# Kernel optimization log

Hardware: AMD Instinct MI355X
Metric: run time of the kernel (lower is better)

## Reference

```python
import jax, jax.numpy as jnp
import numpy as np

N_DRUG, N_CELL, N_GENE = 2048, 2048, 4096
N = N_DRUG + N_CELL + N_GENE
E = 262144
H1, H2, H3, HEADS = 256, 64, 64, 4
N_PAIRS = 10000
EPS = 1e-5


def _gatv2(x, src, dst, Wl, bl, Wr, br, att, bias, heads, out_ch):
    # PyG GATv2Conv: e_ij = att . leaky_relu(Wl x_j + Wr x_i), softmax over incoming edges of i,
    # out_i = sum_j alpha_ij * (Wl x_j), heads concatenated, plus output bias.
    n = x.shape[0]
    xl = (x @ Wl + bl).reshape(n, heads, out_ch)   # source transform
    xr = (x @ Wr + br).reshape(n, heads, out_ch)   # target transform
    e = jax.nn.leaky_relu(xl[src] + xr[dst], 0.2)  # [E, H, C]
    logits = jnp.einsum('ehc,hc->eh', e, att)      # [E, H]
    m = jax.ops.segment_max(logits, dst, num_segments=n)
    ex = jnp.exp(logits - m[dst])
    denom = jax.ops.segment_sum(ex, dst, num_segments=n)
    alpha = ex / denom[dst]                        # [E, H]
    out = jax.ops.segment_sum(xl[src] * alpha[:, :, None], dst, num_segments=n)
    return out.reshape(n, heads * out_ch) + bias, alpha


def _graph_norm(x, gamma, beta, mscale):
    # PyG GraphNorm over a single graph: out = (x - a*mean) / sqrt(var + eps) * gamma + beta
    mu = x.mean(0)
    sub = x - mu * mscale
    var = (sub * sub).mean(0)
    return sub / jnp.sqrt(var + EPS) * gamma + beta


def setup_inputs() -> dict:
    key = jax.random.key(0)
    ks = jax.random.split(key, 24)
    f = jnp.float32
    nrm = lambda k, shape, sc: jax.random.normal(k, shape, f) * sc
    drug = jax.random.normal(ks[0], (N_DRUG, N_DRUG), f)
    cell = jax.random.normal(ks[1], (N_CELL, N_CELL), f)
    gene = jax.random.normal(ks[2], (N_GENE, N_GENE), f)
    # random edges guaranteed to have no self loops (PyG would remove then re-add them)
    src = jax.random.randint(ks[3], (E,), 0, N)
    off = jax.random.randint(ks[4], (E,), 1, N)
    edges = jnp.stack([src, (src + off) % N]).astype(jnp.int32)
    idx_drug = jax.random.randint(ks[5], (N_PAIRS,), 0, N_DRUG)
    idx_cell = N_DRUG + jax.random.randint(ks[6], (N_PAIRS,), 0, N_CELL)
    HC2, HC3 = HEADS * H2, HEADS * H3
    return {
        'drug': drug, 'cell': cell, 'gene': gene,
        'edges': edges, 'idx_drug': idx_drug, 'idx_cell': idx_cell,
        'W_drug': nrm(ks[7], (N_DRUG, H1), 1 / np.sqrt(N_DRUG)), 'b_drug': jnp.zeros((H1,), f),
        'W_cell': nrm(ks[8], (N_CELL, H1), 1 / np.sqrt(N_CELL)), 'b_cell': jnp.zeros((H1,), f),
        'W_gene': nrm(ks[9], (N_GENE, H1), 1 / np.sqrt(N_GENE)), 'b_gene': jnp.zeros((H1,), f),
        'gat1_Wl': nrm(ks[10], (H1, HC2), 1 / np.sqrt(H1)), 'gat1_bl': jnp.zeros((HC2,), f),
        'gat1_Wr': nrm(ks[11], (H1, HC2), 1 / np.sqrt(H1)), 'gat1_br': jnp.zeros((HC2,), f),
        'gat1_att': nrm(ks[12], (HEADS, H2), 1 / np.sqrt(H2)), 'gat1_bias': jnp.zeros((HC2,), f),
        'gat2_Wl': nrm(ks[13], (HC2, HC3), 1 / np.sqrt(HC2)), 'gat2_bl': jnp.zeros((HC3,), f),
        'gat2_Wr': nrm(ks[14], (HC2, HC3), 1 / np.sqrt(HC2)), 'gat2_br': jnp.zeros((HC3,), f),
        'gat2_att': nrm(ks[15], (HEADS, H3), 1 / np.sqrt(H3)), 'gat2_bias': jnp.zeros((HC3,), f),
        'gn1_gamma': jnp.ones((HC2,), f), 'gn1_beta': jnp.zeros((HC2,), f), 'gn1_scale': jnp.ones((HC2,), f),
        'gn2_gamma': jnp.ones((HC3,), f), 'gn2_beta': jnp.zeros((HC3,), f), 'gn2_scale': jnp.ones((HC3,), f),
        'lin1_W': nrm(ks[16], (2 * HC3, 1), 1 / np.sqrt(2 * HC3)), 'lin1_b': jnp.zeros((1,), f),
    }


def reference(drug, cell, gene, edges, idx_drug, idx_cell,
              W_drug, b_drug, W_cell, b_cell, W_gene, b_gene,
              gat1_Wl, gat1_bl, gat1_Wr, gat1_br, gat1_att, gat1_bias,
              gat2_Wl, gat2_bl, gat2_Wr, gat2_br, gat2_att, gat2_bias,
              gn1_gamma, gn1_beta, gn1_scale, gn2_gamma, gn2_beta, gn2_scale,
              lin1_W, lin1_b):
    x = jnp.concatenate([drug @ W_drug + b_drug,
                         cell @ W_cell + b_cell,
                         gene @ W_gene + b_gene], axis=0)  # [N, H1]
    loops = jnp.arange(N, dtype=edges.dtype)
    src = jnp.concatenate([edges[0], loops])  # GATv2Conv adds self loops
    dst = jnp.concatenate([edges[1], loops])
    x, a1 = _gatv2(x, src, dst, gat1_Wl, gat1_bl, gat1_Wr, gat1_br, gat1_att, gat1_bias, HEADS, H2)
    x = jax.nn.relu(_graph_norm(x, gn1_gamma, gn1_beta, gn1_scale))  # dropout = identity (eval)
    x, a2 = _gatv2(x, src, dst, gat2_Wl, gat2_bl, gat2_Wr, gat2_br, gat2_att, gat2_bias, HEADS, H3)
    x = jax.nn.relu(_graph_norm(x, gn2_gamma, gn2_beta, gn2_scale))
    pair = jnp.concatenate([x[idx_drug], x[idx_cell]], axis=1)  # [P, 2*H*H3]
    pred = jax.nn.sigmoid(pair @ lin1_W + lin1_b)
    # get_attention_mat: dense [N,N], every edge position set to the (detached) scalar mean of
    # attention weights; the two layer matrices share edge positions so they simply add.
    val = jax.lax.stop_gradient(a1.mean() + a2.mean())
    attn = jnp.zeros((N, N), x.dtype).at[src, dst].set(val)
    return pred, attn
```

## Files before the change

kernel.cpp:

```cpp
#include <hip/hip_runtime.h>

#define NNODES 8192
#define NEDGE  262144
#define EETOT  270336
#define NPAIRS 10000

typedef __attribute__((ext_vector_type(8))) short s16x8;
typedef __attribute__((ext_vector_type(8))) unsigned short u16x8;
typedef __attribute__((ext_vector_type(4))) float f32x4;

__device__ __forceinline__ float lrelu(float v) { return v > 0.f ? v : 0.2f * v; }

__device__ __forceinline__ void split2(float a, unsigned short& h, unsigned short& l) {
  unsigned u = __float_as_uint(a);
  h = (unsigned short)(u >> 16);
  float hf = __uint_as_float(u & 0xffff0000u);
  float r = a - hf;
  unsigned v = __float_as_uint(r);
  v += 0x7fffu + ((v >> 16) & 1u);
  l = (unsigned short)(v >> 16);
}

__device__ __forceinline__ unsigned short f2bf(float f) {
  unsigned u = __float_as_uint(f);
  u += 0x7fffu + ((u >> 16) & 1u);
  return (unsigned short)(u >> 16);
}
__device__ __forceinline__ float bf2f(unsigned short u) {
  return __uint_as_float((unsigned)u << 16);
}

__device__ __forceinline__ void wsplit_body(const float* __restrict__ W,
    unsigned short* __restrict__ Th, int K, int blk) {
  int col = threadIdx.x;
  int kb = blk * 8;
  u16x8 vh;
#pragma unroll
  for (int i = 0; i < 8; ++i)
    vh[i] = f2bf(W[(size_t)(kb + i) * 256 + col]);
  *(u16x8*)(Th + (size_t)col * K + kb) = vh;
}

__global__ __launch_bounds__(256) void k_wsplit_all(
    const float* __restrict__ Wd, const float* __restrict__ Wc, const float* __restrict__ Wg,
    const float* __restrict__ W1l, const float* __restrict__ W1r,
    const float* __restrict__ W2l, const float* __restrict__ W2r,
    unsigned short* __restrict__ tdh, unsigned short* __restrict__ tch,
    unsigned short* __restrict__ tgh,
    unsigned short* __restrict__ tl1h, unsigned short* __restrict__ tr1h,
    unsigned short* __restrict__ tl2h, unsigned short* __restrict__ tr2h,
    int* __restrict__ counts_d, int* __restrict__ counts_s, float* __restrict__ stats) {
  int b = blockIdx.x;
  if      (b < 256)  wsplit_body(Wd,  tdh, 2048, b);
  else if (b < 512)  wsplit_body(Wc,  tch, 2048, b - 256);
  else if (b < 1024) wsplit_body(Wg,  tgh, 4096, b - 512);
  else if (b < 1056) { wsplit_body(W1l, tl1h, 256, b - 1024);
                       counts_d[(b - 1024) * 256 + threadIdx.x] = 0; }
  else if (b < 1088) { wsplit_body(W1r, tr1h, 256, b - 1056);
                       counts_s[(b - 1056) * 256 + threadIdx.x] = 0; }
  else if (b < 1120) { wsplit_body(W2l, tl2h, 256, b - 1088);
                       if (b < 1092) stats[(b - 1088) * 256 + threadIdx.x] = 0.f; }
  else               wsplit_body(W2r, tr2h, 256, b - 1120);
}

struct Tile128 {
  unsigned short Ah[128][40], Al[128][40], Bh[128][40];
};
struct TileN {
  Tile128 t;
  float nsc[256], nsh[256];
};

template<bool BIAS, bool OUTBF, bool NORM>
__device__ __forceinline__ void gemm_tile128(Tile128& s,
    const float* __restrict__ A, int lda,
    const unsigned short* __restrict__ Th, int ldb, int nsteps,
    const float* __restrict__ bias, float* __restrict__ C,
    unsigned short* __restrict__ Cb,
    const float* __restrict__ nsc, const float* __restrict__ nsh) {
  const int tid = threadIdx.x;
  const int wave = tid >> 6, lane = tid & 63;
  const int g = lane >> 4, r = lane & 15;
  const int wr = (wave >> 1) * 64, wc = (wave & 1) * 64;

  const int ar = tid >> 1, ak = (tid & 1) * 16;
  const float* Arow = A + (size_t)ar * lda + ak;
  const int bc = tid & 127, bk = (tid >> 7) * 16;
  const unsigned short* Bhs = Th + (size_t)bc * ldb + bk;

  f32x4 acc[4][4];
#pragma unroll
  for (int m = 0; m < 4; ++m)
#pragma unroll
    for (int n = 0; n < 4; ++n)
#pragma unroll
      for (int j = 0; j < 4; ++j) acc[m][n][j] = 0.f;

  float4 pa0 = *(const float4*)(Arow);
  float4 pa1 = *(const float4*)(Arow + 4);
  float4 pa2 = *(const float4*)(Arow + 8);
  float4 pa3 = *(const float4*)(Arow + 12);
  u16x8 ph0 = *(const u16x8*)(Bhs);
  u16x8 ph1 = *(const u16x8*)(Bhs + 8);

  for (int t = 0; t < nsteps; ++t) {
    {
      float av[16] = {pa0.x, pa0.y, pa0.z, pa0.w, pa1.x, pa1.y, pa1.z, pa1.w,
                      pa2.x, pa2.y, pa2.z, pa2.w, pa3.x, pa3.y, pa3.z, pa3.w};
      u16x8 vh0, vh1, vl0, vl1;
#pragma unroll
      for (int i = 0; i < 16; ++i) {
        float v = av[i];
        if constexpr (NORM) {
          int ch = t * 32 + ak + i;
          v = fmaxf(v * nsc[ch] + nsh[ch], 0.f);
        }
        unsigned short hh, ll;
        split2(v, hh, ll);
        if (i < 8) { vh0[i] = hh; vl0[i] = ll; }
        else       { vh1[i - 8] = hh; vl1[i - 8] = ll; }
      }
      *(u16x8*)&s.Ah[ar][ak]     = vh0;
      *(u16x8*)&s.Ah[ar][ak + 8] = vh1;
      *(u16x8*)&s.Al[ar][ak]     = vl0;
      *(u16x8*)&s.Al[ar][ak + 8] = vl1;
      *(u16x8*)&s.Bh[bc][bk]     = ph0;
      *(u16x8*)&s.Bh[bc][bk + 8] = ph1;
    }
    __syncthreads();
    if (t + 1 < nsteps) {
      const float* An = Arow + (size_t)(t + 1) * 32;
      pa0 = *(const float4*)(An);
      pa1 = *(const float4*)(An + 4);
      pa2 = *(const float4*)(An + 8);
      pa3 = *(const float4*)(An + 12);
      const unsigned short* Bhn = Bhs + (size_t)(t + 1) * 32;
      ph0 = *(const u16x8*)(Bhn);
      ph1 = *(const u16x8*)(Bhn + 8);
    }
    s16x8 fah[4], fal[4], fbh[4];
#pragma unroll
    for (int m = 0; m < 4; ++m) {
      fah[m] = *(const s16x8*)&s.Ah[wr + m * 16 + r][g * 8];
      fal[m] = *(const s16x8*)&s.Al[wr + m * 16 + r][g * 8];
    }
#pragma unroll
    for (int n = 0; n < 4; ++n)
      fbh[n] = *(const s16x8*)&s.Bh[wc + n * 16 + r][g * 8];
#pragma unroll
    for (int m = 0; m < 4; ++m)
#pragma unroll
      for (int n = 0; n < 4; ++n) {
        acc[m][n] = __builtin_amdgcn_mfma_f32_16x16x32_bf16(fal[m], fbh[n], acc[m][n], 0, 0, 0);
        acc[m][n] = __builtin_amdgcn_mfma_f32_16x16x32_bf16(fah[m], fbh[n], acc[m][n], 0, 0, 0);
      }
    __syncthreads();
  }
#pragma unroll
  for (int m = 0; m < 4; ++m)
#pragma unroll
    for (int n = 0; n < 4; ++n) {
      int col = wc + n * 16 + r;
      float bv = BIAS ? bias[col] : 0.f;
      int rowb = wr + m * 16 + g * 4;
#pragma unroll
      for (int j = 0; j < 4; ++j) {
        float v = acc[m][n][j] + bv;
        if constexpr (OUTBF) Cb[(size_t)(rowb + j) * 256 + col] = f2bf(v);
        else                 C[(size_t)(rowb + j) * 256 + col] = v;
      }
    }
}

#define PDRUG_PLANE ((size_t)2048 * 256)
#define PGENE_PLANE ((size_t)4096 * 256)
__global__ __launch_bounds__(256) void k_inproj_fill(
    const float* __restrict__ drug, const float* __restrict__ cell,
    const float* __restrict__ gene,
    const unsigned short* __restrict__ tdh, const unsigned short* __restrict__ tch,
    const unsigned short* __restrict__ tgh, float* __restrict__ P,
    const int* __restrict__ csrdst, const int* __restrict__ rowst_s,
    float* __restrict__ attn) {
  __shared__ Tile128 s;
  int b = blockIdx.x;
  if (b >= 768) {
    int row = b - 768;
    float* rp = attn + (size_t)row * NNODES;
    f32x4* p4 = (f32x4*)rp;
    f32x4 z = {0.f, 0.f, 0.f, 0.f};
#pragma unroll
    for (int j = 0; j < 8; ++j)
      __builtin_nontemporal_store(z, p4 + j * 256 + threadIdx.x);
    __syncthreads();
    int e0 = rowst_s[row], e1 = rowst_s[row + 1];
    for (int j = e0 + (int)threadIdx.x; j < e1; j += 256)
      rp[csrdst[j]] = 16384.0f / 270336.0f;
    return;
  }
  if (b < 256) {
    int idx = b & 127;
    int colblk = (idx >> 3) & 1;
    int rest = (idx & 7) | ((idx >> 4) << 3);
    int rowblk = rest >> 2, chunk = rest & 3;
    const float* X = (b < 128) ? drug : cell;
    const unsigned short* Th = (b < 128) ? tdh : tch;
    float* Pb = P + ((b < 128) ? 0 : 4 * PDRUG_PLANE);
    gemm_tile128<false, false, false>(s,
        X + (size_t)rowblk * 128 * 2048 + (size_t)chunk * 512, 2048,
        Th + (size_t)colblk * 128 * 2048 + chunk * 512, 2048, 16, nullptr,
        Pb + (size_t)chunk * PDRUG_PLANE + (size_t)rowblk * 128 * 256 + colblk * 128,
        nullptr, nullptr, nullptr);
  } else {
    int idx = b - 256;
    int colblk = (idx >> 3) & 1;
    int rest = (idx & 7) | ((idx >> 4) << 3);
    int rowblk = rest >> 3, chunk = rest & 7;
    gemm_tile128<false, false, false>(s,
        gene + (size_t)rowblk * 128 * 4096 + (size_t)chunk * 512, 4096,
        tgh + (size_t)colblk * 128 * 4096 + chunk * 512, 4096, 16, nullptr,
        P + 8 * PDRUG_PLANE + (size_t)chunk * PGENE_PLANE + (size_t)rowblk * 128 * 256 + colblk * 128,
        nullptr, nullptr, nullptr);
  }
}

__global__ __launch_bounds__(256) void k_reduce(const float* __restrict__ P,
    const float* __restrict__ bd, const float* __restrict__ bc,
    const float* __restrict__ bg, float* __restrict__ out) {
  int idx = blockIdx.x * 256 + threadIdx.x;
  size_t e = (size_t)idx * 4;
  int row = (int)(e >> 8);
  int col = (int)(e & 255);
  const float* base; const float* bias; size_t plane; int np;
  if (row < 2048) {
    base = P + (size_t)row * 256 + col; bias = bd; plane = PDRUG_PLANE; np = 4;
  } else if (row < 4096) {
    base = P + 4 * PDRUG_PLANE + (size_t)(row - 2048) * 256 + col; bias = bc;
    plane = PDRUG_PLANE; np = 4;
  } else {
    base = P + 8 * PDRUG_PLANE + (size_t)(row - 4096) * 256 + col; bias = bg;
    plane = PGENE_PLANE; np = 8;
  }
  float4 s = *(const float4*)(base);
  for (int p = 1; p < np; ++p) {
    float4 v = *(const float4*)(base + p * plane);
    s.x += v.x; s.y += v.y; s.z += v.z; s.w += v.w;
  }
  float4 bv = *(const float4*)(bias + col);
  s.x += bv.x; s.y += bv.y; s.z += bv.z; s.w += bv.w;
  *(float4*)(out + e) = s;
}

template<bool NORM>
__global__ __launch_bounds__(256) void k_gemm2(const float* __restrict__ A,
    const unsigned short* __restrict__ ThL, const unsigned short* __restrict__ ThR,
    const float* __restrict__ biasL, const float* __restrict__ biasR,
    unsigned short* __restrict__ CLb, float* __restrict__ CR,
    const float* __restrict__ csum, const float* __restrict__ csumsq,
    const float* __restrict__ gamma, const float* __restrict__ beta,
    const float* __restrict__ mscale) {
  __shared__ TileN s;
  int b = blockIdx.x;
  int sub = (b >> 3) & 3;
  int x = (b & 7) | ((b >> 5) << 3);
  if constexpr (NORM) {
    int c = threadIdx.x;
    float mu = csum[c] * (1.0f / 8192.0f);
    float ex2 = csumsq[c] * (1.0f / 8192.0f);
    float smu = mscale[c] * mu;
    float var = ex2 - 2.f * smu * mu + smu * smu;
    float sc = rsqrtf(var + 1e-5f) * gamma[c];
    s.nsc[c] = sc;
    s.nsh[c] = beta[c] - smu * sc;
    __syncthreads();
  }
  int row0 = x * 128;
  int col0 = (sub & 1) * 128;
  if (sub >= 2) {
    gemm_tile128<true, false, NORM>(s.t, A + (size_t)row0 * 256, 256,
        ThR + (size_t)col0 * 256, 256, 8,
        biasR + col0, CR + (size_t)row0 * 256 + col0, nullptr, s.nsc, s.nsh);
  } else {
    gemm_tile128<true, true, NORM>(s.t, A + (size_t)row0 * 256, 256,
        ThL + (size_t)col0 * 256, 256, 8,
        biasL + col0, nullptr, CLb + (size_t)row0 * 256 + col0, s.nsc, s.nsh);
  }
}

__global__ void k_count2(const int* __restrict__ edges, int* __restrict__ cd,
                         int* __restrict__ cs) {
  int e = blockIdx.x * blockDim.x + threadIdx.x;
  if (e >= EETOT) return;
  int s, d;
  if (e < NEDGE) { s = edges[e]; d = edges[NEDGE + e]; } else { s = d = e - NEDGE; }
  atomicAdd(&cd[d], 1);
  atomicAdd(&cs[s], 1);
}

__global__ __launch_bounds__(1024) void k_scan2(
    const int* __restrict__ c0, int* __restrict__ r0, int* __restrict__ u0,
    const int* __restrict__ c1, int* __restrict__ r1, int* __restrict__ u1) {
  const int* counts = blockIdx.x ? c1 : c0;
  int* row_start = blockIdx.x ? r1 : r0;
  int* cursor = blockIdx.x ? u1 : u0;
  __shared__ int part[1024];
  int t = threadIdx.x;
  int base = t * 8;
  int loc[8];
  int s = 0;
#pragma unroll
  for (int j = 0; j < 8; ++j) { loc[j] = s; s += counts[base + j]; }
  part[t] = s;
  __syncthreads();
  for (int off = 1; off < 1024; off <<= 1) {
    int v = (t >= off) ? part[t - off] : 0;
    __syncthreads();
    part[t] += v;
    __syncthreads();
  }
  int pre = (t == 0) ? 0 : part[t - 1];
#pragma unroll
  for (int j = 0; j < 8; ++j) {
    int v = pre + loc[j];
    row_start[base + j] = v;
    cursor[base + j] = v;
  }
  if (t == 1023) row_start[NNODES] = pre + s;
}

__global__ void k_place2(const int* __restrict__ edges, int* __restrict__ curd,
    int* __restrict__ curs, int* __restrict__ csrsrc, int* __restrict__ csrdst) {
  int e = blockIdx.x * blockDim.x + threadIdx.x;
  if (e >= EETOT) return;
  int s, d;
  if (e < NEDGE) { s = edges[e]; d = edges[NEDGE + e]; } else { s = d = e - NEDGE; }
  int pd = atomicAdd(&curd[d], 1);
  csrsrc[pd] = s;
  int ps = atomicAdd(&curs[s], 1);
  csrdst[ps] = d;
}

__global__ __launch_bounds__(256) void k_gat(
    const unsigned short* __restrict__ xl, const float* __restrict__ xr,
    const float* __restrict__ att, const int* __restrict__ csrsrc,
    const int* __restrict__ row_start, const float* __restrict__ bias,
    float* __restrict__ out) {
  int i = blockIdx.x * 4 + (threadIdx.x >> 6);
  int lane = threadIdx.x & 63;
  int co = (lane >> 4) * 64 + (lane & 15) * 4;
  float4 w4 = *(const float4*)(att + co);
  float4 r4 = *(const float4*)(xr + (size_t)i * 256 + co);
  float sum = 0.f, ax = 0.f, ay = 0.f, az = 0.f, aw = 0.f;
  int e0 = row_start[i], e1 = row_start[i + 1];
  int deg = e1 - e0;

  for (int cb = 0; cb < deg; cb += 64) {
    int cn = min(deg - cb, 64);
    int myid = (lane < cn) ? csrsrc[e0 + cb + lane] : 0;
    auto g = [&](int j) {
      int s = __shfl(myid, j);
      return *(const ushort4*)(xl + (size_t)s * 256 + co);
    };
    ushort4 c0, c1, c2, c3, n0, n1, n2, n3;
    int curn = min(cn, 4);
    int p = 0;
    if (curn > 0) c0 = g(0);
    if (curn > 1) c1 = g(1);
    if (curn > 2) c2 = g(2);
    if (curn > 3) c3 = g(3);
    p = curn;
    for (;;) {
      int nxtn = min(cn - p, 4);
      if (nxtn > 0) n0 = g(p);
      if (nxtn > 1) n1 = g(p + 1);
      if (nxtn > 2) n2 = g(p + 2);
      if (nxtn > 3) n3 = g(p + 3);
#pragma unroll
      for (int j = 0; j < 4; ++j) {
        if (j >= curn) break;
        ushort4 u = (j == 0) ? c0 : (j == 1) ? c1 : (j == 2) ? c2 : c3;
        float x0 = bf2f(u.x), x1 = bf2f(u.y), x2 = bf2f(u.z), x3 = bf2f(u.w);
        float t = w4.x * lrelu(x0 + r4.x) + w4.y * lrelu(x1 + r4.y) +
                  w4.z * lrelu(x2 + r4.z) + w4.w * lrelu(x3 + r4.w);
        t += __shfl_xor(t, 1);
        t += __shfl_xor(t, 2);
        t += __shfl_xor(t, 4);
        t += __shfl_xor(t, 8);
        float el = __expf(fminf(t, 60.f));
        sum += el;
        ax += el * x0; ay += el * x1; az += el * x2; aw += el * x3;
      }
      if (nxtn <= 0) break;
      c0 = n0; c1 = n1; c2 = n2; c3 = n3;
      curn = nxtn; p += nxtn;
    }
  }
  float inv = 1.0f / sum;
  float4 bv = *(const float4*)(bias + co);
  float4 r;
  r.x = ax * inv + bv.x; r.y = ay * inv + bv.y;
  r.z = az * inv + bv.z; r.w = aw * inv + bv.w;
  *(float4*)(out + (size_t)i * 256 + co) = r;
}

__global__ __launch_bounds__(256) void k_colstats(const float* __restrict__ x,
    float* __restrict__ csum, float* __restrict__ csumsq) {
  int c = threadIdx.x;
  int r0 = blockIdx.x * 32;
  float s = 0.f, s2 = 0.f;
  for (int r = 0; r < 32; ++r) {
    float v = x[(size_t)(r0 + r) * 256 + c];
    s += v; s2 += v * v;
  }
  atomicAdd(&csum[c], s);
  atomicAdd(&csumsq[c], s2);
}

__global__ __launch_bounds__(256) void k_pred(const float* __restrict__ h,
    const int* __restrict__ idx_drug, const int* __restrict__ idx_cell,
    const float* __restrict__ W, const float* __restrict__ b,
    const float* __restrict__ csum, const float* __restrict__ csumsq,
    const float* __restrict__ gamma, const float* __restrict__ beta,
    const float* __restrict__ mscale, float* __restrict__ out) {
  int p = blockIdx.x * 4 + (threadIdx.x >> 6);
  if (p >= NPAIRS) return;
  int lane = threadIdx.x & 63;
  int rd = idx_drug[p], rc = idx_cell[p];
  float4 a  = *(const float4*)(h + (size_t)rd * 256 + lane * 4);
  float4 cg = *(const float4*)(h + (size_t)rc * 256 + lane * 4);
  float4 wa = *(const float4*)(W + lane * 4);
  float4 wc = *(const float4*)(W + 256 + lane * 4);
  float av[4] = {a.x, a.y, a.z, a.w};
  float cv[4] = {cg.x, cg.y, cg.z, cg.w};
  float wv[4] = {wa.x, wa.y, wa.z, wa.w};
  float uv[4] = {wc.x, wc.y, wc.z, wc.w};
  float t = 0.f;
#pragma unroll
  for (int j = 0; j < 4; ++j) {
    int ch = lane * 4 + j;
    float mu = csum[ch] * (1.0f / 8192.0f);
    float ex2 = csumsq[ch] * (1.0f / 8192.0f);
    float smu = mscale[ch] * mu;
    float var = ex2 - 2.f * smu * mu + smu * smu;
    float sc = rsqrtf(var + 1e-5f) * gamma[ch];
    float sh = beta[ch] - smu * sc;
    t += fmaxf(av[j] * sc + sh, 0.f) * wv[j] + fmaxf(cv[j] * sc + sh, 0.f) * uv[j];
  }
#pragma unroll
  for (int off = 1; off < 64; off <<= 1) t += __shfl_xor(t, off);
  if (lane == 0) out[p] = 1.0f / (1.0f + __expf(-(t + b[0])));
}

extern "C" void kernel_launch(void* const* d_in, const int* in_sizes, int n_in,
                              void* d_out, int out_size, void* d_ws, size_t ws_size,
                              hipStream_t stream) {
  const float* drug = (const float*)d_in[0];
  const float* cell = (const float*)d_in[1];
  const float* gene = (const float*)d_in[2];
  const int*   edges = (const int*)d_in[3];
  const int*   idxd = (const int*)d_in[4];
  const int*   idxc = (const int*)d_in[5];
  const float* Wd = (const float*)d_in[6];   const float* bd = (const float*)d_in[7];
  const float* Wc = (const float*)d_in[8];   const float* bc = (const float*)d_in[9];
  const float* Wg = (const float*)d_in[10];  const float* bg = (const float*)d_in[11];
  const float* g1Wl = (const float*)d_in[12]; const float* g1bl = (const float*)d_in[13];
  const float* g1Wr = (const float*)d_in[14]; const float* g1br = (const float*)d_in[15];
  const float* g1att = (const float*)d_in[16]; const float* g1bias = (const float*)d_in[17];
  const float* g2Wl = (const float*)d_in[18]; const float* g2bl = (const float*)d_in[19];
  const float* g2Wr = (const float*)d_in[20]; const float* g2br = (const float*)d_in[21];
  const float* g2att = (const float*)d_in[22]; const float* g2bias = (const float*)d_in[23];
  const float* gn1g = (const float*)d_in[24]; const float* gn1b = (const float*)d_in[25];
  const float* gn1s = (const float*)d_in[26];
  const float* gn2g = (const float*)d_in[27]; const float* gn2b = (const float*)d_in[28];
  const float* gn2s = (const float*)d_in[29];
  const float* linW = (const float*)d_in[30]; const float* linb = (const float*)d_in[31];
  float* out = (float*)d_out;
  (void)in_sizes; (void)n_in; (void)out_size; (void)ws_size;

  char* ws = (char*)d_ws;
  size_t off = 0;
  auto take = [&](size_t bytes) -> void* {
    void* p = ws + off;
    off += (bytes + 255) & ~(size_t)255;
    return p;
  };
  float* bufA = (float*)take((size_t)NNODES * 256 * 4);
  unsigned short* bufBb = (unsigned short*)take((size_t)NNODES * 256 * 2);
  float* bufC = (float*)take((size_t)NNODES * 256 * 4);
  int* counts_d = (int*)take((size_t)NNODES * 4);
  int* counts_s = (int*)take((size_t)NNODES * 4);
  float* stats  = (float*)take(4 * 256 * 4);
  int* rowst_d  = (int*)take((size_t)(NNODES + 1) * 4);
  int* rowst_s  = (int*)take((size_t)(NNODES + 1) * 4);
  int* cursor_d = (int*)take((size_t)NNODES * 4);
  int* cursor_s = (int*)take((size_t)NNODES * 4);
  int* csrsrc   = (int*)take((size_t)EETOT * 4);
  int* csrdst   = (int*)take((size_t)EETOT * 4);
  unsigned short* tdh = (unsigned short*)take((size_t)256 * 2048 * 2);
  unsigned short* tch = (unsigned short*)take((size_t)256 * 2048 * 2);
  unsigned short* tgh = (unsigned short*)take((size_t)256 * 4096 * 2);
  unsigned short* tl1h = (unsigned short*)take((size_t)256 * 256 * 2);
  unsigned short* tr1h = (unsigned short*)take((size_t)256 * 256 * 2);
  unsigned short* tl2h = (unsigned short*)take((size_t)256 * 256 * 2);
  unsigned short* tr2h = (unsigned short*)take((size_t)256 * 256 * 2);
  float* Ppart = (float*)take((8 * PDRUG_PLANE + 8 * PGENE_PLANE) * 4);

  k_wsplit_all<<<1152, 256, 0, stream>>>(Wd, Wc, Wg, g1Wl, g1Wr, g2Wl, g2Wr,
      tdh, tch, tgh, tl1h, tr1h, tl2h, tr2h, counts_d, counts_s, stats);

  k_count2<<<EETOT / 256, 256, 0, stream>>>(edges, counts_d, counts_s);
  k_scan2<<<2, 1024, 0, stream>>>(counts_d, rowst_d, cursor_d, counts_s, rowst_s, cursor_s);
  k_place2<<<EETOT / 256, 256, 0, stream>>>(edges, cursor_d, cursor_s, csrsrc, csrdst);

  k_inproj_fill<<<768 + NNODES, 256, 0, stream>>>(drug, cell, gene, tdh, tch, tgh,
      Ppart, csrdst, rowst_s, out + NPAIRS);
  k_reduce<<<NNODES * 256 / 4 / 256, 256, 0, stream>>>(Ppart, bd, bc, bg, bufA);

  k_gemm2<false><<<256, 256, 0, stream>>>(bufA, tl1h, tr1h, g1bl, g1br,
      bufBb, bufC, nullptr, nullptr, nullptr, nullptr, nullptr);
  k_gat<<<NNODES / 4, 256, 0, stream>>>(bufBb, bufC, g1att, csrsrc, rowst_d, g1bias, bufA);
  k_colstats<<<NNODES / 32, 256, 0, stream>>>(bufA, stats, stats + 256);

  k_gemm2<true><<<256, 256, 0, stream>>>(bufA, tl2h, tr2h, g2bl, g2br,
      bufBb, bufC, stats, stats + 256, gn1g, gn1b, gn1s);
  k_gat<<<NNODES / 4, 256, 0, stream>>>(bufBb, bufC, g2att, csrsrc, rowst_d, g2bias, bufA);
  k_colstats<<<NNODES / 32, 256, 0, stream>>>(bufA, stats + 512, stats + 768);

  k_pred<<<NPAIRS / 4, 256, 0, stream>>>(bufA, idxd, idxc, linW, linb,
      stats + 512, stats + 768, gn2g, gn2b, gn2s, out);
}
```

Measured before the change: 294.4 us.

## Halve gene split-K chunks and deepen GAT gather prefetch to eight

The gene input-projection GEMM now uses four split-K chunks of 1024 instead of eight chunks of 512. This halves its block count and the partial-sum planes that k_reduce must read and sum, and lets the reduce loop run a fixed, unrolled four iterations. Separately, the GAT edge loop now prefetches eight neighbour rows per batch instead of four, giving more loads in flight. The costs are fewer blocks, and so less parallelism, in the gene GEMM, plus higher register pressure in k_gat.

New measurement: 296.6 us. Within noise of the previous version (+0.7%).

```diff
diff --git a/kernel.cpp b/kernel.cpp
--- a/kernel.cpp
+++ b/kernel.cpp
@@ -183,8 +183,8 @@
     float* __restrict__ attn) {
   __shared__ Tile128 s;
   int b = blockIdx.x;
-  if (b >= 768) {
-    int row = b - 768;
+  if (b >= 512) {
+    int row = b - 512;
     float* rp = attn + (size_t)row * NNODES;
     f32x4* p4 = (f32x4*)rp;
     f32x4 z = {0.f, 0.f, 0.f, 0.f};
@@ -214,10 +214,10 @@
     int idx = b - 256;
     int colblk = (idx >> 3) & 1;
     int rest = (idx & 7) | ((idx >> 4) << 3);
-    int rowblk = rest >> 3, chunk = rest & 7;
+    int rowblk = rest >> 2, chunk = rest & 3;
     gemm_tile128<false, false, false>(s,
-        gene + (size_t)rowblk * 128 * 4096 + (size_t)chunk * 512, 4096,
-        tgh + (size_t)colblk * 128 * 4096 + chunk * 512, 4096, 16, nullptr,
+        gene + (size_t)rowblk * 128 * 4096 + (size_t)chunk * 1024, 4096,
+        tgh + (size_t)colblk * 128 * 4096 + chunk * 1024, 4096, 32, nullptr,
         P + 8 * PDRUG_PLANE + (size_t)chunk * PGENE_PLANE + (size_t)rowblk * 128 * 256 + colblk * 128,
         nullptr, nullptr, nullptr);
   }
@@ -230,18 +230,19 @@
   size_t e = (size_t)idx * 4;
   int row = (int)(e >> 8);
   int col = (int)(e & 255);
-  const float* base; const float* bias; size_t plane; int np;
+  const float* base; const float* bias; size_t plane;
   if (row < 2048) {
-    base = P + (size_t)row * 256 + col; bias = bd; plane = PDRUG_PLANE; np = 4;
+    base = P + (size_t)row * 256 + col; bias = bd; plane = PDRUG_PLANE;
   } else if (row < 4096) {
     base = P + 4 * PDRUG_PLANE + (size_t)(row - 2048) * 256 + col; bias = bc;
-    plane = PDRUG_PLANE; np = 4;
+    plane = PDRUG_PLANE;
   } else {
     base = P + 8 * PDRUG_PLANE + (size_t)(row - 4096) * 256 + col; bias = bg;
-    plane = PGENE_PLANE; np = 8;
+    plane = PGENE_PLANE;
   }
   float4 s = *(const float4*)(base);
-  for (int p = 1; p < np; ++p) {
+#pragma unroll
+  for (int p = 1; p < 4; ++p) {
     float4 v = *(const float4*)(base + p * plane);
     s.x += v.x; s.y += v.y; s.z += v.z; s.w += v.w;
   }
@@ -360,24 +361,21 @@
       int s = __shfl(myid, j);
       return *(const ushort4*)(xl + (size_t)s * 256 + co);
     };
-    ushort4 c0, c1, c2, c3, n0, n1, n2, n3;
-    int curn = min(cn, 4);
-    int p = 0;
-    if (curn > 0) c0 = g(0);
-    if (curn > 1) c1 = g(1);
-    if (curn > 2) c2 = g(2);
-    if (curn > 3) c3 = g(3);
-    p = curn;
+    ushort4 cur[8], nxt[8];
+    int curn = min(cn, 8);
+#pragma unroll
+    for (int j = 0; j < 8; ++j)
+      if (j < curn) cur[j] = g(j);
+    int p = curn;
     for (;;) {
-      int nxtn = min(cn - p, 4);
-      if (nxtn > 0) n0 = g(p);
-      if (nxtn > 1) n1 = g(p + 1);
-      if (nxtn > 2) n2 = g(p + 2);
-      if (nxtn > 3) n3 = g(p + 3);
-#pragma unroll
-      for (int j = 0; j < 4; ++j) {
+      int nxtn = min(cn - p, 8);
+#pragma unroll
+      for (int j = 0; j < 8; ++j)
+        if (j < nxtn) nxt[j] = g(p + j);
+#pragma unroll
+      for (int j = 0; j < 8; ++j) {
         if (j >= curn) break;
-        ushort4 u = (j == 0) ? c0 : (j == 1) ? c1 : (j == 2) ? c2 : c3;
+        ushort4 u = cur[j];
         float x0 = bf2f(u.x), x1 = bf2f(u.y), x2 = bf2f(u.z), x3 = bf2f(u.w);
         float t = w4.x * lrelu(x0 + r4.x) + w4.y * lrelu(x1 + r4.y) +
                   w4.z * lrelu(x2 + r4.z) + w4.w * lrelu(x3 + r4.w);
@@ -390,7 +388,8 @@
         ax += el * x0; ay += el * x1; az += el * x2; aw += el * x3;
       }
       if (nxtn <= 0) break;
-      c0 = n0; c1 = n1; c2 = n2; c3 = n3;
+#pragma unroll
+      for (int j = 0; j < 8; ++j) cur[j] = nxt[j];
       curn = nxtn; p += nxtn;
     }
   }
@@ -502,7 +501,7 @@
   unsigned short* tr1h = (unsigned short*)take((size_t)256 * 256 * 2);
   unsigned short* tl2h = (unsigned short*)take((size_t)256 * 256 * 2);
   unsigned short* tr2h = (unsigned short*)take((size_t)256 * 256 * 2);
-  float* Ppart = (float*)take((8 * PDRUG_PLANE + 8 * PGENE_PLANE) * 4);
+  float* Ppart = (float*)take((8 * PDRUG_PLANE + 4 * PGENE_PLANE) * 4);
 
   k_wsplit_all<<<1152, 256, 0, stream>>>(Wd, Wc, Wg, g1Wl, g1Wr, g2Wl, g2Wr,
       tdh, tch, tgh, tl1h, tr1h, tl2h, tr2h, counts_d, counts_s, stats);
@@ -511,7 +510,7 @@
   k_scan2<<<2, 1024, 0, stream>>>(counts_d, rowst_d, cursor_d, counts_s, rowst_s, cursor_s);
   k_place2<<<EETOT / 256, 256, 0, stream>>>(edges, cursor_d, cursor_s, csrsrc, csrdst);
 
-  k_inproj_fill<<<768 + NNODES, 256, 0, stream>>>(drug, cell, gene, tdh, tch, tgh,
+  k_inproj_fill<<<512 + NNODES, 256, 0, stream>>>(drug, cell, gene, tdh, tch, tgh,
       Ppart, csrdst, rowst_s, out + NPAIRS);
   k_reduce<<<NNODES * 256 / 4 / 256, 256, 0, stream>>>(Ppart, bd, bc, bg, bufA);
 
```
